# Performance work log

Hardware: AMD Instinct MI355X
Metric: run time of the kernel (lower is better)

## Reference

```python
import jax, jax.numpy as jnp
import numpy as np

B, T, D = 2, 2048, 1024
H, KVH, HD = 16, 4, 64  # query heads, kv heads, head_dim
GROUPS = H // KVH


def apply_rope(x, cos, sin):
    # x: (B, nh, T, hd); cos/sin: (max_T, hd//2)
    t = x.shape[2]
    c = cos[:t][None, None]  # (1,1,T,hd//2)
    s = sin[:t][None, None]
    half = x.shape[-1] // 2
    x1, x2 = x[..., :half], x[..., half:]
    rotated = jnp.concatenate((-x2, x1), axis=-1)
    cf = jnp.concatenate((c, c), axis=-1)  # repeat(1,1,1,2)
    sf = jnp.concatenate((s, s), axis=-1)
    return x * cf + rotated * sf


def setup_inputs():
    key = jax.random.key(0)
    ks = jax.random.split(key, 5)
    x = jax.random.normal(ks[0], (B, T, D), dtype=jnp.float32)
    # RoPE tables: theta^(-i/half) frequencies
    half = HD // 2
    inv_freq = 1.0 / (10000.0 ** (jnp.arange(half, dtype=jnp.float32) / half))
    ang = jnp.arange(T, dtype=jnp.float32)[:, None] * inv_freq[None, :]  # (T, half)
    rope_cos = jnp.cos(ang)
    rope_sin = jnp.sin(ang)
    # Causal additive mask
    causal = jnp.tril(jnp.ones((T, T), dtype=bool))
    attention_mask = jnp.where(causal, 0.0, -1e9).astype(jnp.float32)[None, None]
    scale = 0.02
    Wq = jax.random.normal(ks[1], (D, D), dtype=jnp.float32) * scale
    Wk = jax.random.normal(ks[2], (D, KVH * HD), dtype=jnp.float32) * scale
    Wv = jax.random.normal(ks[3], (D, KVH * HD), dtype=jnp.float32) * scale
    Wo = jax.random.normal(ks[4], (D, D), dtype=jnp.float32) * scale
    return {"x": x, "rope_cos": rope_cos, "rope_sin": rope_sin,
            "attention_mask": attention_mask,
            "Wq": Wq, "Wk": Wk, "Wv": Wv, "Wo": Wo}


def reference(x, rope_cos, rope_sin, attention_mask, Wq, Wk, Wv, Wo):
    b, t, _ = x.shape
    q = (x @ Wq).reshape(b, t, H, HD).transpose(0, 2, 1, 3)      # (B,H,T,hd)
    k = (x @ Wk).reshape(b, t, KVH, HD).transpose(0, 2, 1, 3)    # (B,KVH,T,hd)
    v = (x @ Wv).reshape(b, t, KVH, HD).transpose(0, 2, 1, 3)
    q = apply_rope(q, rope_cos, rope_sin)
    k = apply_rope(k, rope_cos, rope_sin)
    if GROUPS > 1:
        k = jnp.repeat(k, GROUPS, axis=1)  # repeat_interleave over heads
        v = jnp.repeat(v, GROUPS, axis=1)
    scale = 1.0 / np.sqrt(HD)
    attn = jnp.einsum('bhqd,bhkd->bhqk', q, k) * scale
    attn = attn + attention_mask
    attn = jax.nn.softmax(attn.astype(jnp.float32), axis=-1).astype(q.dtype)
    out = jnp.einsum('bhqk,bhkd->bhqd', attn, v)
    out = out.transpose(0, 2, 1, 3).reshape(b, t, D)
    return out @ Wo
```

## Files before the change

kernel.cpp:

```cpp
#include <hip/hip_runtime.h>

typedef __attribute__((ext_vector_type(8))) short short8;
typedef __attribute__((ext_vector_type(4))) short short4v;
typedef __attribute__((ext_vector_type(4))) float f32x4;

#define T_ 2048
#define H_ 16
#define KVH_ 4
#define QSCALE 0.18033688011112042f
#define DEFER 8.0f

__device__ inline unsigned short f2bf(float f) {
    unsigned u = __builtin_bit_cast(unsigned, f);
    u += 0x7fff + ((u >> 16) & 1);
    return (unsigned short)(u >> 16);
}
__device__ inline float bf2f(unsigned short v) {
    unsigned u = ((unsigned)v) << 16;
    return __builtin_bit_cast(float, u);
}

__device__ inline void gl_lds16(const unsigned short* g, unsigned short* lds) {
    __builtin_amdgcn_global_load_lds(
        (const __attribute__((address_space(1))) unsigned int*)g,
        (__attribute__((address_space(3))) unsigned int*)lds, 16, 0, 0);
}

__global__ void cast_bf16(const float* __restrict__ in,
                          unsigned short* __restrict__ out, int n8) {
    int i = blockIdx.x * blockDim.x + threadIdx.x;
    if (i >= n8) return;
    float4 v0 = ((const float4*)in)[i * 2];
    float4 v1 = ((const float4*)in)[i * 2 + 1];
    short8 o;
    o[0] = f2bf(v0.x); o[1] = f2bf(v0.y); o[2] = f2bf(v0.z); o[3] = f2bf(v0.w);
    o[4] = f2bf(v1.x); o[5] = f2bf(v1.y); o[6] = f2bf(v1.z); o[7] = f2bf(v1.w);
    ((short8*)out)[i] = o;
}

__global__ __launch_bounds__(256) void transpose_cast(
        const float* __restrict__ W, unsigned short* __restrict__ out,
        int K, int N, int rowoff) {
    __shared__ unsigned short ts[64][66];
    const int bx = blockIdx.x, by = blockIdx.y, tid = threadIdx.x;
    #pragma unroll
    for (int s = 0; s < 16; ++s) {
        int idx = tid + s * 256;
        int kl = idx >> 6, nl = idx & 63;
        ts[kl][nl] = f2bf(W[(size_t)(by * 64 + kl) * N + bx * 64 + nl]);
    }
    __syncthreads();
    #pragma unroll
    for (int s = 0; s < 16; ++s) {
        int idx = tid + s * 256;
        int nl = idx >> 6, kl = idx & 63;
        out[(size_t)(rowoff + bx * 64 + nl) * K + by * 64 + kl] = ts[kl][nl];
    }
}

template <int MODE>
__global__ __launch_bounds__(256) void gemm_mfma(
        const unsigned short* __restrict__ A,
        const unsigned short* __restrict__ Bt,
        void* __restrict__ Cq, unsigned short* __restrict__ Ck,
        unsigned short* __restrict__ Cvt,
        const float* __restrict__ rc, const float* __restrict__ rs,
        int M, int N, int K) {
    __shared__ __align__(16) unsigned short As[128 * 32];
    __shared__ __align__(16) unsigned short Bs[64 * 32];
    const int tid = threadIdx.x;
    const int w = tid >> 6, l = tid & 63, lk = l & 15, lg = l >> 4;
    const int bx = blockIdx.x, by = blockIdx.y;

    const unsigned short* Arow = A + (size_t)by * 128 * K;
    const unsigned short* Brow = Bt + (size_t)bx * 64 * K;

    f32x4 acc[2][4];
    #pragma unroll
    for (int m = 0; m < 2; ++m)
        #pragma unroll
        for (int n = 0; n < 4; ++n) acc[m][n] = (f32x4){0, 0, 0, 0};

    for (int k0 = 0; k0 < K; k0 += 32) {
        #pragma unroll
        for (int p = 0; p < 2; ++p) {
            int cb = p * 256 + w * 64;
            int c = cb + l;
            int row = c >> 2, ko = (c & 3) * 8;
            gl_lds16(Arow + (size_t)row * K + k0 + ko, As + cb * 8);
        }
        {
            int c = w * 64 + l;
            int row = c >> 2, ko = (c & 3) * 8;
            gl_lds16(Brow + (size_t)row * K + k0 + ko, Bs + c * 8);
        }
        __syncthreads();
        short8 aF[2], bF[4];
        #pragma unroll
        for (int m = 0; m < 2; ++m)
            aF[m] = *(const short8*)&As[(w * 32 + m * 16 + lk) * 32 + lg * 8];
        #pragma unroll
        for (int n = 0; n < 4; ++n)
            bF[n] = *(const short8*)&Bs[(n * 16 + lk) * 32 + lg * 8];
        #pragma unroll
        for (int m = 0; m < 2; ++m)
            #pragma unroll
            for (int n = 0; n < 4; ++n)
                acc[m][n] = __builtin_amdgcn_mfma_f32_16x16x32_bf16(
                    aF[m], bF[n], acc[m][n], 0, 0, 0);
        __syncthreads();
    }

    const int rowbase = by * 128 + w * 32;
    if constexpr (MODE == 0) {
        float* C = (float*)Cq;
        #pragma unroll
        for (int m = 0; m < 2; ++m)
            #pragma unroll
            for (int r = 0; r < 4; ++r) {
                size_t ro = (size_t)(rowbase + m * 16 + lg * 4 + r) * N + bx * 64 + lk;
                #pragma unroll
                for (int n = 0; n < 4; ++n) C[ro + n * 16] = acc[m][n][r];
            }
    }
    if constexpr (MODE == 1) {
        const int colgrp = bx;
        if (colgrp < 16) {
            unsigned short* C = (unsigned short*)Cq;
            const int h = colgrp;
            #pragma unroll
            for (int m = 0; m < 2; ++m)
                #pragma unroll
                for (int r = 0; r < 4; ++r) {
                    int trow = rowbase + m * 16 + lg * 4 + r;
                    int b = trow >> 11, t = trow & (T_ - 1);
                    size_t ob = (((size_t)(b * 16 + h)) * T_ + t) * 64;
                    #pragma unroll
                    for (int n = 0; n < 2; ++n) {
                        int d = n * 16 + lk;
                        float cc = rc[t * 32 + d], ss = rs[t * 32 + d];
                        float x1 = acc[m][n][r], x2 = acc[m][n + 2][r];
                        C[ob + d]      = f2bf((x1 * cc - x2 * ss) * QSCALE);
                        C[ob + d + 32] = f2bf((x2 * cc + x1 * ss) * QSCALE);
                    }
                }
        } else if (colgrp < 20) {
            const int kvh = colgrp - 16;
            #pragma unroll
            for (int m = 0; m < 2; ++m)
                #pragma unroll
                for (int r = 0; r < 4; ++r) {
                    int trow = rowbase + m * 16 + lg * 4 + r;
                    int b = trow >> 11, t = trow & (T_ - 1);
                    size_t ob = (((size_t)(b * 4 + kvh)) * T_ + t) * 64;
                    #pragma unroll
                    for (int n = 0; n < 2; ++n) {
                        int d = n * 16 + lk;
                        float cc = rc[t * 32 + d], ss = rs[t * 32 + d];
                        float x1 = acc[m][n][r], x2 = acc[m][n + 2][r];
                        Ck[ob + d]      = f2bf(x1 * cc - x2 * ss);
                        Ck[ob + d + 32] = f2bf(x2 * cc + x1 * ss);
                    }
                }
        } else {
            const int kvh = colgrp - 20;
            #pragma unroll
            for (int m = 0; m < 2; ++m) {
                int trow0 = rowbase + m * 16 + lg * 4;
                int b = trow0 >> 11, t0 = trow0 & (T_ - 1);
                #pragma unroll
                for (int n = 0; n < 4; ++n) {
                    int d = n * 16 + lk;
                    short4v pk;
                    #pragma unroll
                    for (int r = 0; r < 4; ++r) pk[r] = f2bf(acc[m][n][r]);
                    *(short4v*)(Cvt + (((size_t)(b * 4 + kvh)) * 64 + d) * T_ + t0) = pk;
                }
            }
        }
    }
}

#define SWC(row, col) ((col) ^ (((row) & 7) << 3))

__global__ __launch_bounds__(256) void attn_mfma(
        const unsigned short* __restrict__ Q,
        const unsigned short* __restrict__ K,
        const unsigned short* __restrict__ Vt,
        unsigned short* __restrict__ O,
        float* __restrict__ PM, float* __restrict__ PLp,
        unsigned short* __restrict__ PACC) {
    __shared__ __align__(16) unsigned short Ks[2][64 * 64];
    __shared__ __align__(16) unsigned short Vs[2][64 * 64];
    __shared__ __align__(16) unsigned short Pl[4][32 * 64];

    const int bid = blockIdx.x;
    int bh, qt, kt0, ktend, ck;
    bool direct;
    if (bid < 256) {
        bh = bid & 31; qt = 8 + (bid >> 5);
        kt0 = 0; ktend = 16; ck = 0; direct = false;
    } else if (bid < 512) {
        int j = bid - 256;
        bh = j & 31; qt = 7 - (j >> 5);
        kt0 = 0; ktend = 2 * qt + 2; ck = 0; direct = true;
    } else {
        int j = bid - 512;
        bh = j & 31; qt = 15 - (j >> 5);
        kt0 = 16; ktend = 2 * qt + 2; ck = 1; direct = false;
    }
    const int nkt = ktend - kt0;
    const int h = bh & 15, b = bh >> 4, kv = h >> 2;
    const int tid = threadIdx.x;
    const int w = tid >> 6, l = tid & 63;
    const int lk = l & 15, lg = l >> 4;

    const unsigned short* Kb = K + ((size_t)(b * 4 + kv)) * T_ * 64;
    const unsigned short* Vb = Vt + ((size_t)(b * 4 + kv)) * 64 * T_;

    short8 af[2][2];
    #pragma unroll
    for (int m = 0; m < 2; ++m) {
        const unsigned short* qp =
            Q + (((size_t)(b * 16 + h)) * T_ + qt * 128 + w * 32 + m * 16 + lk) * 64 + lg * 8;
        af[m][0] = *(const short8*)(qp);
        af[m][1] = *(const short8*)(qp + 32);
    }

    f32x4 acc[2][4];
    f32x4 lacc[2];
    float mrow[2][4];
    #pragma unroll
    for (int m = 0; m < 2; ++m) {
        lacc[m] = (f32x4){0, 0, 0, 0};
        #pragma unroll
        for (int db = 0; db < 4; ++db) acc[m][db] = (f32x4){0, 0, 0, 0};
        #pragma unroll
        for (int r = 0; r < 4; ++r) mrow[m][r] = -1e38f;
    }

    short8 ones;
    #pragma unroll
    for (int i = 0; i < 8; ++i) ones[i] = (short)0x3F80;

    const int sr = l >> 3;
    const int sg = l & 7;
    auto stage = [&](int buf, int kt) {
        #pragma unroll
        for (int p = 0; p < 2; ++p) {
            const int ch = w * 2 + p;
            const int row = ch * 8 + sr;
            const int gs = (sg ^ sr) * 8;
            gl_lds16(Kb + ((size_t)(kt * 64 + row)) * 64 + gs, &Ks[buf][ch * 512]);
            gl_lds16(Vb + (size_t)row * T_ + kt * 64 + gs,     &Vs[buf][ch * 512]);
        }
    };

    stage(0, kt0);
    for (int i = 0; i < nkt; ++i) {
        const int kt = kt0 + i;
        const int cur = i & 1;
        __syncthreads();
        if (i + 1 < nkt) stage(cur ^ 1, kt0 + i + 1);

        float s4[2][4][4];
        __builtin_amdgcn_s_setprio(1);
        #pragma unroll
        for (int nt = 0; nt < 4; ++nt) {
            const int row = nt * 16 + lk;
            short8 b0 = *(const short8*)&Ks[cur][row * 64 + SWC(row, lg * 8)];
            short8 b1 = *(const short8*)&Ks[cur][row * 64 + SWC(row, 32 + lg * 8)];
            f32x4 c0 = {0, 0, 0, 0}, c1 = {0, 0, 0, 0};
            c0 = __builtin_amdgcn_mfma_f32_16x16x32_bf16(af[0][0], b0, c0, 0, 0, 0);
            c1 = __builtin_amdgcn_mfma_f32_16x16x32_bf16(af[1][0], b0, c1, 0, 0, 0);
            c0 = __builtin_amdgcn_mfma_f32_16x16x32_bf16(af[0][1], b1, c0, 0, 0, 0);
            c1 = __builtin_amdgcn_mfma_f32_16x16x32_bf16(af[1][1], b1, c1, 0, 0, 0);
            #pragma unroll
            for (int r = 0; r < 4; ++r) { s4[0][nt][r] = c0[r]; s4[1][nt][r] = c1[r]; }
        }
        __builtin_amdgcn_s_setprio(0);

        if (kt >= 2 * qt) {
            #pragma unroll
            for (int m = 0; m < 2; ++m) {
                const int qg = qt * 128 + w * 32 + m * 16 + lg * 4;
                #pragma unroll
                for (int nt = 0; nt < 4; ++nt) {
                    const int kg = kt * 64 + nt * 16 + lk;
                    #pragma unroll
                    for (int r = 0; r < 4; ++r)
                        if (kg > qg + r) s4[m][nt][r] = -1e30f;
                }
            }
        }

        float lm[2][4];
        bool need = false;
        #pragma unroll
        for (int m = 0; m < 2; ++m)
            #pragma unroll
            for (int r = 0; r < 4; ++r) {
                lm[m][r] = fmaxf(fmaxf(s4[m][0][r], s4[m][1][r]),
                                 fmaxf(s4[m][2][r], s4[m][3][r]));
                need = need || (lm[m][r] > mrow[m][r] + DEFER);
            }
        if (__any(need)) {
            #pragma unroll
            for (int m = 0; m < 2; ++m)
                #pragma unroll
                for (int r = 0; r < 4; ++r) {
                    float v = lm[m][r];
                    v = fmaxf(v, __shfl_xor(v, 1));
                    v = fmaxf(v, __shfl_xor(v, 2));
                    v = fmaxf(v, __shfl_xor(v, 4));
                    v = fmaxf(v, __shfl_xor(v, 8));
                    float nm = fmaxf(mrow[m][r], v);
                    float corr = exp2f(mrow[m][r] - nm);
                    mrow[m][r] = nm;
                    #pragma unroll
                    for (int db = 0; db < 4; ++db) acc[m][db][r] *= corr;
                    lacc[m][r] *= corr;
                }
        }
        #pragma unroll
        for (int m = 0; m < 2; ++m)
            #pragma unroll
            for (int r = 0; r < 4; ++r)
                #pragma unroll
                for (int nt = 0; nt < 4; ++nt)
                    s4[m][nt][r] = exp2f(s4[m][nt][r] - mrow[m][r]);

        #pragma unroll
        for (int m = 0; m < 2; ++m)
            #pragma unroll
            for (int nt = 0; nt < 4; ++nt)
                #pragma unroll
                for (int r = 0; r < 4; ++r) {
                    const int row = m * 16 + lg * 4 + r;
                    Pl[w][row * 64 + SWC(row, nt * 16 + lk)] = f2bf(s4[m][nt][r]);
                }

        __builtin_amdgcn_s_setprio(1);
        #pragma unroll
        for (int kk = 0; kk < 2; ++kk) {
            const int pr0 = lk, pr1 = 16 + lk;
            short8 pa0 = *(const short8*)&Pl[w][pr0 * 64 + SWC(pr0, kk * 32 + lg * 8)];
            short8 pa1 = *(const short8*)&Pl[w][pr1 * 64 + SWC(pr1, kk * 32 + lg * 8)];
            lacc[0] = __builtin_amdgcn_mfma_f32_16x16x32_bf16(pa0, ones, lacc[0], 0, 0, 0);
            lacc[1] = __builtin_amdgcn_mfma_f32_16x16x32_bf16(pa1, ones, lacc[1], 0, 0, 0);
            #pragma unroll
            for (int db = 0; db < 4; ++db) {
                const int vrow = db * 16 + lk;
                short8 vb = *(const short8*)&Vs[cur][vrow * 64 + SWC(vrow, kk * 32 + lg * 8)];
                acc[0][db] = __builtin_amdgcn_mfma_f32_16x16x32_bf16(pa0, vb, acc[0][db], 0, 0, 0);
                acc[1][db] = __builtin_amdgcn_mfma_f32_16x16x32_bf16(pa1, vb, acc[1][db], 0, 0, 0);
            }
        }
        __builtin_amdgcn_s_setprio(0);
    }

    if (direct) {
        #pragma unroll
        for (int m = 0; m < 2; ++m)
            #pragma unroll
            for (int r = 0; r < 4; ++r) {
                float inv = 1.f / lacc[m][r];
                int t = qt * 128 + w * 32 + m * 16 + lg * 4 + r;
                #pragma unroll
                for (int db = 0; db < 4; ++db)
                    O[(((size_t)(b * T_ + t)) * 16 + h) * 64 + db * 16 + lk] =
                        f2bf(acc[m][db][r] * inv);
            }
    } else {
        const int p = ((bh << 3) + (qt - 8)) * 2 + ck;
        #pragma unroll
        for (int m = 0; m < 2; ++m)
            #pragma unroll
            for (int r = 0; r < 4; ++r) {
                const int row = w * 32 + m * 16 + lg * 4 + r;
                if (lk == 0) {
                    PM[p * 128 + row]  = mrow[m][r];
                    PLp[p * 128 + row] = lacc[m][r];
                }
                #pragma unroll
                for (int db = 0; db < 4; ++db)
                    PACC[((size_t)p * 128 + row) * 64 + db * 16 + lk] = f2bf(acc[m][db][r]);
            }
    }
}

__global__ __launch_bounds__(256) void combine_attn(
        const float* __restrict__ PM, const float* __restrict__ PLp,
        const unsigned short* __restrict__ PACC,
        unsigned short* __restrict__ O) {
    const int cid = blockIdx.x;
    const int bh = cid & 31, qt = 8 + (cid >> 5);
    const int h = bh & 15, b = bh >> 4;
    const int tid = threadIdx.x;
    const int row = tid >> 1, cg = (tid & 1) * 32;
    const int p0 = ((bh << 3) + (qt - 8)) * 2, p1 = p0 + 1;

    float mA = PM[p0 * 128 + row], mB = PM[p1 * 128 + row];
    float lA = PLp[p0 * 128 + row], lB = PLp[p1 * 128 + row];
    float M = fmaxf(mA, mB);
    float wA = exp2f(mA - M), wB = exp2f(mB - M);
    float inv = 1.f / (lA * wA + lB * wB);
    wA *= inv; wB *= inv;

    const unsigned short* a = &PACC[((size_t)p0 * 128 + row) * 64 + cg];
    const unsigned short* c = &PACC[((size_t)p1 * 128 + row) * 64 + cg];
    int t = qt * 128 + row;
    unsigned short* op = &O[(((size_t)(b * T_ + t)) * 16 + h) * 64 + cg];
    #pragma unroll
    for (int j = 0; j < 4; ++j) {
        short8 va = *(const short8*)(a + j * 8);
        short8 vb = *(const short8*)(c + j * 8);
        short8 o;
        #pragma unroll
        for (int i = 0; i < 8; ++i)
            o[i] = f2bf(bf2f((unsigned short)va[i]) * wA +
                        bf2f((unsigned short)vb[i]) * wB);
        *(short8*)(op + j * 8) = o;
    }
}

extern "C" void kernel_launch(void* const* d_in, const int* in_sizes, int n_in,
                              void* d_out, int out_size, void* d_ws, size_t ws_size,
                              hipStream_t stream) {
    const float* x  = (const float*)d_in[0];
    const float* rc = (const float*)d_in[1];
    const float* rs = (const float*)d_in[2];
    const float* Wq = (const float*)d_in[4];
    const float* Wk = (const float*)d_in[5];
    const float* Wv = (const float*)d_in[6];
    const float* Wo = (const float*)d_in[7];
    float* out = (float*)d_out;

    unsigned short* ws = (unsigned short*)d_ws;
    unsigned short* xb  = ws;
    unsigned short* Wt  = ws + 4194304;
    unsigned short* Wot = ws + 5767168;
    unsigned short* Qbf = ws + 6815744;
    unsigned short* Kbf = ws + 11010048;
    unsigned short* Vtb = ws + 12058624;
    unsigned short* Ob  = ws + 13107200;

    float* PM            = (float*)d_ws;
    float* PLp           = PM + 512 * 128;
    unsigned short* PACC = (unsigned short*)(PLp + 512 * 128);

    dim3 blk(256);
    cast_bf16<<<2048, blk, 0, stream>>>(x, xb, 524288);
    transpose_cast<<<dim3(16, 16), blk, 0, stream>>>(Wq, Wt, 1024, 1024, 0);
    transpose_cast<<<dim3(4, 16),  blk, 0, stream>>>(Wk, Wt, 1024, 256, 1024);
    transpose_cast<<<dim3(4, 16),  blk, 0, stream>>>(Wv, Wt, 1024, 256, 1280);
    transpose_cast<<<dim3(16, 16), blk, 0, stream>>>(Wo, Wot, 1024, 1024, 0);

    gemm_mfma<1><<<dim3(24, 32), blk, 0, stream>>>(
        xb, Wt, (void*)Qbf, Kbf, Vtb, rc, rs, 4096, 1536, 1024);

    attn_mfma<<<dim3(768), blk, 0, stream>>>(Qbf, Kbf, Vtb, Ob, PM, PLp, PACC);
    combine_attn<<<dim3(256), blk, 0, stream>>>(PM, PLp, PACC, Ob);

    gemm_mfma<0><<<dim3(16, 32), blk, 0, stream>>>(
        Ob, Wot, (void*)out, nullptr, nullptr, nullptr, nullptr, 4096, 1024, 1024);
}
```

Measured before the change: 126.0 us.

## Switch attention to 32x32x16 MFMA with transposed S and register-resident P

Restructures the attention inner loop to compute S^T with 32x32x16 bf16 MFMAs, so each lane owns one query row's softmax state. P is packed to bf16 with v_cvt_pk_bf16_f32 and permlane32_swap directly into MFMA operand layout, which removes the LDS round-trip for P and the ones-vector MFMA used to form row sums. Row max and sum now use a single cross-half shuffle. The trade-offs are more shuffles when rescaling the output accumulators and scalar 2-byte output stores in the epilogue.

Result: faster. 120.0 us (-4.7%).

```diff
diff --git a/kernel.cpp b/kernel.cpp
--- a/kernel.cpp
+++ b/kernel.cpp
@@ -3,6 +3,9 @@
 typedef __attribute__((ext_vector_type(8))) short short8;
 typedef __attribute__((ext_vector_type(4))) short short4v;
 typedef __attribute__((ext_vector_type(4))) float f32x4;
+typedef __attribute__((ext_vector_type(16))) float f32x16;
+typedef __attribute__((ext_vector_type(2))) unsigned uint2v;
+typedef __attribute__((ext_vector_type(4))) unsigned uint4v;
 
 #define T_ 2048
 #define H_ 16
@@ -18,6 +21,11 @@
 __device__ inline float bf2f(unsigned short v) {
     unsigned u = ((unsigned)v) << 16;
     return __builtin_bit_cast(float, u);
+}
+__device__ inline unsigned pk2(float lo, float hi) {
+    unsigned r;
+    asm("v_cvt_pk_bf16_f32 %0, %1, %2" : "=v"(r) : "v"(lo), "v"(hi));
+    return r;
 }
 
 __device__ inline void gl_lds16(const unsigned short* g, unsigned short* lds) {
@@ -182,6 +190,7 @@
 }
 
 #define SWC(row, col) ((col) ^ (((row) & 7) << 3))
+#define CROW(r, hi) (((r) & 3) + 8 * ((r) >> 2) + 4 * (hi))
 
 __global__ __launch_bounds__(256) void attn_mfma(
         const unsigned short* __restrict__ Q,
@@ -192,7 +201,6 @@
         unsigned short* __restrict__ PACC) {
     __shared__ __align__(16) unsigned short Ks[2][64 * 64];
     __shared__ __align__(16) unsigned short Vs[2][64 * 64];
-    __shared__ __align__(16) unsigned short Pl[4][32 * 64];
 
     const int bid = blockIdx.x;
     int bh, qt, kt0, ktend, ck;
@@ -213,38 +221,25 @@
     const int h = bh & 15, b = bh >> 4, kv = h >> 2;
     const int tid = threadIdx.x;
     const int w = tid >> 6, l = tid & 63;
-    const int lk = l & 15, lg = l >> 4;
+    const int q32 = l & 31, hi = l >> 5;
 
     const unsigned short* Kb = K + ((size_t)(b * 4 + kv)) * T_ * 64;
     const unsigned short* Vb = Vt + ((size_t)(b * 4 + kv)) * 64 * T_;
 
-    short8 af[2][2];
+    short8 qf[4];
+    {
+        const unsigned short* qp =
+            Q + (((size_t)(b * 16 + h)) * T_ + qt * 128 + w * 32 + q32) * 64 + hi * 8;
+        #pragma unroll
+        for (int s = 0; s < 4; ++s) qf[s] = *(const short8*)(qp + 16 * s);
+    }
+
+    f32x16 o0, o1;
     #pragma unroll
-    for (int m = 0; m < 2; ++m) {
-        const unsigned short* qp =
-            Q + (((size_t)(b * 16 + h)) * T_ + qt * 128 + w * 32 + m * 16 + lk) * 64 + lg * 8;
-        af[m][0] = *(const short8*)(qp);
-        af[m][1] = *(const short8*)(qp + 32);
-    }
-
-    f32x4 acc[2][4];
-    f32x4 lacc[2];
-    float mrow[2][4];
-    #pragma unroll
-    for (int m = 0; m < 2; ++m) {
-        lacc[m] = (f32x4){0, 0, 0, 0};
-        #pragma unroll
-        for (int db = 0; db < 4; ++db) acc[m][db] = (f32x4){0, 0, 0, 0};
-        #pragma unroll
-        for (int r = 0; r < 4; ++r) mrow[m][r] = -1e38f;
-    }
-
-    short8 ones;
-    #pragma unroll
-    for (int i = 0; i < 8; ++i) ones[i] = (short)0x3F80;
-
-    const int sr = l >> 3;
-    const int sg = l & 7;
+    for (int i = 0; i < 16; ++i) { o0[i] = 0.f; o1[i] = 0.f; }
+    float mloc = -1e38f, lsum = 0.f;
+
+    const int sr = l >> 3, sg = l & 7;
     auto stage = [&](int buf, int kt) {
         #pragma unroll
         for (int p = 0; p < 2; ++p) {
@@ -256,6 +251,19 @@
         }
     };
 
+    auto mk = [&](float e0, float e1, float e2, float e3,
+                  float e4, float e5, float e6, float e7) -> short8 {
+        unsigned a0 = pk2(e0, e1);
+        unsigned b0 = pk2(e4, e5);
+        uint2v r02 = __builtin_amdgcn_permlane32_swap(a0, b0, false, false);
+        unsigned a1 = pk2(e2, e3);
+        unsigned b1 = pk2(e6, e7);
+        uint2v r13 = __builtin_amdgcn_permlane32_swap(a1, b1, false, false);
+        uint4v u;
+        u[0] = r02[0]; u[1] = r13[0]; u[2] = r02[1]; u[3] = r13[1];
+        return __builtin_bit_cast(short8, u);
+    };
+
     stage(0, kt0);
     for (int i = 0; i < nkt; ++i) {
         const int kt = kt0 + i;
@@ -263,129 +271,101 @@
         __syncthreads();
         if (i + 1 < nkt) stage(cur ^ 1, kt0 + i + 1);
 
-        float s4[2][4][4];
+        f32x16 st0, st1;
+        #pragma unroll
+        for (int r = 0; r < 16; ++r) { st0[r] = 0.f; st1[r] = 0.f; }
         __builtin_amdgcn_s_setprio(1);
         #pragma unroll
-        for (int nt = 0; nt < 4; ++nt) {
-            const int row = nt * 16 + lk;
-            short8 b0 = *(const short8*)&Ks[cur][row * 64 + SWC(row, lg * 8)];
-            short8 b1 = *(const short8*)&Ks[cur][row * 64 + SWC(row, 32 + lg * 8)];
-            f32x4 c0 = {0, 0, 0, 0}, c1 = {0, 0, 0, 0};
-            c0 = __builtin_amdgcn_mfma_f32_16x16x32_bf16(af[0][0], b0, c0, 0, 0, 0);
-            c1 = __builtin_amdgcn_mfma_f32_16x16x32_bf16(af[1][0], b0, c1, 0, 0, 0);
-            c0 = __builtin_amdgcn_mfma_f32_16x16x32_bf16(af[0][1], b1, c0, 0, 0, 0);
-            c1 = __builtin_amdgcn_mfma_f32_16x16x32_bf16(af[1][1], b1, c1, 0, 0, 0);
-            #pragma unroll
-            for (int r = 0; r < 4; ++r) { s4[0][nt][r] = c0[r]; s4[1][nt][r] = c1[r]; }
+        for (int s = 0; s < 4; ++s) {
+            const int c = 16 * s + hi * 8;
+            const int kr0 = q32, kr1 = 32 + q32;
+            short8 k0 = *(const short8*)&Ks[cur][kr0 * 64 + SWC(kr0, c)];
+            short8 k1 = *(const short8*)&Ks[cur][kr1 * 64 + SWC(kr1, c)];
+            st0 = __builtin_amdgcn_mfma_f32_32x32x16_bf16(k0, qf[s], st0, 0, 0, 0);
+            st1 = __builtin_amdgcn_mfma_f32_32x32x16_bf16(k1, qf[s], st1, 0, 0, 0);
         }
         __builtin_amdgcn_s_setprio(0);
 
         if (kt >= 2 * qt) {
-            #pragma unroll
-            for (int m = 0; m < 2; ++m) {
-                const int qg = qt * 128 + w * 32 + m * 16 + lg * 4;
-                #pragma unroll
-                for (int nt = 0; nt < 4; ++nt) {
-                    const int kg = kt * 64 + nt * 16 + lk;
-                    #pragma unroll
-                    for (int r = 0; r < 4; ++r)
-                        if (kg > qg + r) s4[m][nt][r] = -1e30f;
-                }
+            const int qg = qt * 128 + w * 32 + q32;
+            #pragma unroll
+            for (int r = 0; r < 16; ++r) {
+                const int kg = kt * 64 + CROW(r, hi);
+                if (kg > qg)      st0[r] = -1e30f;
+                if (kg + 32 > qg) st1[r] = -1e30f;
             }
         }
 
-        float lm[2][4];
-        bool need = false;
-        #pragma unroll
-        for (int m = 0; m < 2; ++m)
-            #pragma unroll
-            for (int r = 0; r < 4; ++r) {
-                lm[m][r] = fmaxf(fmaxf(s4[m][0][r], s4[m][1][r]),
-                                 fmaxf(s4[m][2][r], s4[m][3][r]));
-                need = need || (lm[m][r] > mrow[m][r] + DEFER);
+        float pm = st0[0];
+        #pragma unroll
+        for (int r = 1; r < 16; ++r) pm = fmaxf(pm, st0[r]);
+        #pragma unroll
+        for (int r = 0; r < 16; ++r) pm = fmaxf(pm, st1[r]);
+        pm = fmaxf(pm, __shfl_xor(pm, 32));
+
+        if (__any(pm > mloc + DEFER)) {
+            const float nm = fmaxf(mloc, pm);
+            const float corr = exp2f(mloc - nm);
+            mloc = nm;
+            lsum *= corr;
+            #pragma unroll
+            for (int r = 0; r < 16; ++r) {
+                const float cr = __shfl(corr, CROW(r, hi));
+                o0[r] *= cr;
+                o1[r] *= cr;
             }
-        if (__any(need)) {
-            #pragma unroll
-            for (int m = 0; m < 2; ++m)
-                #pragma unroll
-                for (int r = 0; r < 4; ++r) {
-                    float v = lm[m][r];
-                    v = fmaxf(v, __shfl_xor(v, 1));
-                    v = fmaxf(v, __shfl_xor(v, 2));
-                    v = fmaxf(v, __shfl_xor(v, 4));
-                    v = fmaxf(v, __shfl_xor(v, 8));
-                    float nm = fmaxf(mrow[m][r], v);
-                    float corr = exp2f(mrow[m][r] - nm);
-                    mrow[m][r] = nm;
-                    #pragma unroll
-                    for (int db = 0; db < 4; ++db) acc[m][db][r] *= corr;
-                    lacc[m][r] *= corr;
-                }
-        }
-        #pragma unroll
-        for (int m = 0; m < 2; ++m)
-            #pragma unroll
-            for (int r = 0; r < 4; ++r)
-                #pragma unroll
-                for (int nt = 0; nt < 4; ++nt)
-                    s4[m][nt][r] = exp2f(s4[m][nt][r] - mrow[m][r]);
-
-        #pragma unroll
-        for (int m = 0; m < 2; ++m)
-            #pragma unroll
-            for (int nt = 0; nt < 4; ++nt)
-                #pragma unroll
-                for (int r = 0; r < 4; ++r) {
-                    const int row = m * 16 + lg * 4 + r;
-                    Pl[w][row * 64 + SWC(row, nt * 16 + lk)] = f2bf(s4[m][nt][r]);
-                }
+        }
+
+        float ls = 0.f;
+        #pragma unroll
+        for (int r = 0; r < 16; ++r) {
+            st0[r] = exp2f(st0[r] - mloc); ls += st0[r];
+            st1[r] = exp2f(st1[r] - mloc); ls += st1[r];
+        }
+        ls += __shfl_xor(ls, 32);
+        lsum += ls;
+
+        short8 pa0 = mk(st0[0], st0[1], st0[2],  st0[3],  st0[4],  st0[5],  st0[6],  st0[7]);
+        short8 pa1 = mk(st0[8], st0[9], st0[10], st0[11], st0[12], st0[13], st0[14], st0[15]);
+        short8 pa2 = mk(st1[0], st1[1], st1[2],  st1[3],  st1[4],  st1[5],  st1[6],  st1[7]);
+        short8 pa3 = mk(st1[8], st1[9], st1[10], st1[11], st1[12], st1[13], st1[14], st1[15]);
 
         __builtin_amdgcn_s_setprio(1);
-        #pragma unroll
-        for (int kk = 0; kk < 2; ++kk) {
-            const int pr0 = lk, pr1 = 16 + lk;
-            short8 pa0 = *(const short8*)&Pl[w][pr0 * 64 + SWC(pr0, kk * 32 + lg * 8)];
-            short8 pa1 = *(const short8*)&Pl[w][pr1 * 64 + SWC(pr1, kk * 32 + lg * 8)];
-            lacc[0] = __builtin_amdgcn_mfma_f32_16x16x32_bf16(pa0, ones, lacc[0], 0, 0, 0);
-            lacc[1] = __builtin_amdgcn_mfma_f32_16x16x32_bf16(pa1, ones, lacc[1], 0, 0, 0);
-            #pragma unroll
-            for (int db = 0; db < 4; ++db) {
-                const int vrow = db * 16 + lk;
-                short8 vb = *(const short8*)&Vs[cur][vrow * 64 + SWC(vrow, kk * 32 + lg * 8)];
-                acc[0][db] = __builtin_amdgcn_mfma_f32_16x16x32_bf16(pa0, vb, acc[0][db], 0, 0, 0);
-                acc[1][db] = __builtin_amdgcn_mfma_f32_16x16x32_bf16(pa1, vb, acc[1][db], 0, 0, 0);
-            }
+        const int vd0 = q32, vd1 = 32 + q32;
+        #pragma unroll
+        for (int ks = 0; ks < 4; ++ks) {
+            short8 paf = (ks == 0) ? pa0 : (ks == 1) ? pa1 : (ks == 2) ? pa2 : pa3;
+            const int c = 16 * ks + hi * 8;
+            short8 vb0 = *(const short8*)&Vs[cur][vd0 * 64 + SWC(vd0, c)];
+            short8 vb1 = *(const short8*)&Vs[cur][vd1 * 64 + SWC(vd1, c)];
+            o0 = __builtin_amdgcn_mfma_f32_32x32x16_bf16(paf, vb0, o0, 0, 0, 0);
+            o1 = __builtin_amdgcn_mfma_f32_32x32x16_bf16(paf, vb1, o1, 0, 0, 0);
         }
         __builtin_amdgcn_s_setprio(0);
     }
 
     if (direct) {
         #pragma unroll
-        for (int m = 0; m < 2; ++m)
-            #pragma unroll
-            for (int r = 0; r < 4; ++r) {
-                float inv = 1.f / lacc[m][r];
-                int t = qt * 128 + w * 32 + m * 16 + lg * 4 + r;
-                #pragma unroll
-                for (int db = 0; db < 4; ++db)
-                    O[(((size_t)(b * T_ + t)) * 16 + h) * 64 + db * 16 + lk] =
-                        f2bf(acc[m][db][r] * inv);
-            }
+        for (int r = 0; r < 16; ++r) {
+            const float inv = 1.f / __shfl(lsum, CROW(r, hi));
+            const int t = qt * 128 + w * 32 + CROW(r, hi);
+            unsigned short* op = &O[(((size_t)(b * T_ + t)) * 16 + h) * 64 + q32];
+            op[0]  = f2bf(o0[r] * inv);
+            op[32] = f2bf(o1[r] * inv);
+        }
     } else {
         const int p = ((bh << 3) + (qt - 8)) * 2 + ck;
-        #pragma unroll
-        for (int m = 0; m < 2; ++m)
-            #pragma unroll
-            for (int r = 0; r < 4; ++r) {
-                const int row = w * 32 + m * 16 + lg * 4 + r;
-                if (lk == 0) {
-                    PM[p * 128 + row]  = mrow[m][r];
-                    PLp[p * 128 + row] = lacc[m][r];
-                }
-                #pragma unroll
-                for (int db = 0; db < 4; ++db)
-                    PACC[((size_t)p * 128 + row) * 64 + db * 16 + lk] = f2bf(acc[m][db][r]);
-            }
+        if (l < 32) {
+            PM[p * 128 + w * 32 + l]  = mloc;
+            PLp[p * 128 + w * 32 + l] = lsum;
+        }
+        #pragma unroll
+        for (int r = 0; r < 16; ++r) {
+            const int row = w * 32 + CROW(r, hi);
+            unsigned short* pp = &PACC[((size_t)p * 128 + row) * 64 + q32];
+            pp[0]  = f2bf(o0[r]);
+            pp[32] = f2bf(o1[r]);
+        }
     }
 }
 
```
